# Optimization experiments

Hardware: AMD Instinct MI355X
Metric: run time of the kernel (lower is better)

The kernel has to match this reference:

```python
import jax, jax.numpy as jnp
import numpy as np

B, N, C, R = 16, 1024, 256, 8
E = 262144
NUM_SUPER = 32
EPS = 1e-5


def _ln(x, g, b):
    mu = jnp.mean(x, axis=-1, keepdims=True)
    var = jnp.var(x, axis=-1, keepdims=True)
    return (x - mu) / jnp.sqrt(var + EPS) * g + b


def setup_inputs() -> dict:
    key = jax.random.key(0)
    ks = jax.random.split(key, 20)

    def w(k, shape, fan_in):
        return (jax.random.normal(k, shape, jnp.float32) / np.sqrt(fan_in)).astype(jnp.float32)

    return dict(
        x=jax.random.normal(ks[0], (B, N, C), jnp.float32),
        batch_edge_index=jax.random.randint(ks[1], (2, E), 0, B * N),
        batch_edge_types=jax.random.randint(ks[2], (E,), 0, R),
        # cross-modal attention
        Wq=w(ks[3], (C, C), C), bq=jnp.zeros((C,), jnp.float32),
        Wk=w(ks[4], (C, C), C), bk=jnp.zeros((C,), jnp.float32),
        Wv=w(ks[5], (C, C), C), bv=jnp.zeros((C,), jnp.float32),
        Wg=w(ks[6], (2 * C, C), 2 * C), bg=jnp.zeros((C,), jnp.float32),
        ln_attn_g=jnp.ones((C,), jnp.float32), ln_attn_b=jnp.zeros((C,), jnp.float32),
        # confidence net
        Wc1=w(ks[7], (C, C // 2), C), bc1=jnp.zeros((C // 2,), jnp.float32),
        Wc2=w(ks[8], (C // 2, 1), C // 2), bc2=jnp.zeros((1,), jnp.float32),
        # feature mixer
        Wm=w(ks[9], (2 * C, C), 2 * C), bm=jnp.zeros((C,), jnp.float32),
        ln1_g=jnp.ones((C,), jnp.float32), ln1_b=jnp.zeros((C,), jnp.float32),
        # RGCN
        W_rel=w(ks[10], (R, C, C), C),
        W_root=w(ks[11], (C, C), C),
        b_rgcn=jnp.zeros((C,), jnp.float32),
        ln2_g=jnp.ones((C,), jnp.float32), ln2_b=jnp.zeros((C,), jnp.float32),
        # super class head
        Wh=w(ks[12], (C, NUM_SUPER), C), bh=jnp.zeros((NUM_SUPER,), jnp.float32),
    )


def reference(x, batch_edge_index, batch_edge_types,
              Wq, bq, Wk, bk, Wv, bv, Wg, bg, ln_attn_g, ln_attn_b,
              Wc1, bc1, Wc2, bc2, Wm, bm, ln1_g, ln1_b,
              W_rel, W_root, b_rgcn, ln2_g, ln2_b, Wh, bh):
    residual = x
    q = x @ Wq + bq
    k = x @ Wk + bk
    v = x @ Wv + bv
    attn = jax.nn.softmax(jnp.einsum('bnc,bmc->bnm', q, k) / jnp.sqrt(jnp.float32(C)), axis=-1)
    out = jnp.einsum('bnm,bmc->bnc', attn, v)
    gate = jax.nn.sigmoid(jnp.concatenate([out, residual], axis=-1) @ Wg + bg)
    validated = _ln(gate * out + (1.0 - gate) * residual, ln_attn_g, ln_attn_b)

    conf = jax.nn.sigmoid(jax.nn.relu(validated @ Wc1 + bc1) @ Wc2 + bc2)  # [B,N,1]
    weighted = validated * conf
    xm = jax.nn.relu(jnp.concatenate([x, weighted], axis=-1) @ Wm + bm)
    xn = _ln(xm, ln1_g, ln1_b).reshape(B * N, C)

    # RGCNConv (PyG defaults: mean aggregation per relation, root weight, bias)
    src, dst = batch_edge_index[0], batch_edge_index[1]
    h = jnp.einsum('nc,rcd->rnd', xn, W_rel)          # [R, B*N, C] relation-transformed nodes
    msg = h[batch_edge_types, src]                    # [E, C] per-edge gather
    seg = dst * R + batch_edge_types                  # (node, relation) segment id
    cnt = jax.ops.segment_sum(jnp.ones((E,), xn.dtype), seg, num_segments=B * N * R)
    msg = msg / jnp.maximum(cnt[seg], 1.0)[:, None]
    agg = jax.ops.segment_sum(msg, dst, num_segments=B * N)
    x_rgcn = agg + xn @ W_root + b_rgcn
    x_rgcn = jax.nn.relu(_ln(x_rgcn.reshape(B, N, C), ln2_g, ln2_b))

    denom = jnp.maximum(conf.sum(axis=1), 1e-8)       # [B,1]
    pooled = (x_rgcn * conf).sum(axis=1) / denom      # [B,C]
    return pooled @ Wh + bh                           # [B, NUM_SUPER]
```

## Files before the change

### kernel.cpp

```cpp
#include <hip/hip_runtime.h>
#include <hip/hip_bf16.h>

#define B_ 16
#define N_ 1024
#define C_ 256
#define R_ 8
#define E_ 262144
#define NS_ 32
#define BN_ (B_*N_)
#define BNC_ (BN_*C_)

typedef __hip_bfloat16 bf16;
typedef __attribute__((ext_vector_type(4))) float f32x4;
typedef __attribute__((ext_vector_type(8))) short bf16x8;

__device__ __forceinline__ float b2f(bf16 x) { return __bfloat162float(x); }
__device__ __forceinline__ bf16  f2b(float x) { return __float2bfloat16(x); }
__device__ __forceinline__ float us2f(unsigned short u) { return __uint_as_float((unsigned)u << 16); }

__device__ __forceinline__ void gload16(const void* g, void* l) {
    auto gp = (const __attribute__((address_space(1))) void*)(unsigned long long)g;
    auto lp = (__attribute__((address_space(3))) void*)(unsigned)(unsigned long long)l;
    __builtin_amdgcn_global_load_lds(gp, lp, 16, 0, 0);
}

template<int ACT>
__global__ __launch_bounds__(256) void gemm_bf16(
    const bf16* __restrict__ A, int lda, long long sA,
    const bf16* __restrict__ Bm, int ldb, long long sB,
    bf16* __restrict__ Cc, int ldc, long long sC,
    const float* __restrict__ bias, const float* __restrict__ bias2,
    const float* __restrict__ bias3, int K)
{
    __shared__ short sbuf[16384];
    const int tid = threadIdx.x;
    const int lane = tid & 63, w = tid >> 6;
    const int wr = w >> 1, wc = w & 1;
    const int bm = blockIdx.y * 128, bn = blockIdx.x * 128;
    const bf16* Ab = A + (size_t)blockIdx.z * sA;
    const bf16* Bb = Bm + (size_t)blockIdx.z * sB;
    bf16* Cb = Cc + (size_t)blockIdx.z * sC;

    const int rg = lane >> 2;
    const int kswz = ((lane & 3) ^ ((rg >> 1) & 3)) * 8;

    f32x4 acc[4][4];
    const f32x4 zz = {0.f, 0.f, 0.f, 0.f};
    #pragma unroll
    for (int i = 0; i < 4; ++i)
        #pragma unroll
        for (int j = 0; j < 4; ++j) acc[i][j] = zz;

    const int fr = lane & 15;
    const int fm = lane >> 4;
    const int fslot = (fm ^ ((fr >> 1) & 3)) * 8;

    const int NI = K >> 5;

#define STAGE_AB(bi, kk) do {                                                          \
    _Pragma("unroll")                                                                  \
    for (int t_ = 0; t_ < 2; ++t_) {                                                   \
        gload16(Ab + (size_t)(bm + t_*64 + w*16 + rg) * lda + (kk) + kswz,             \
                sbuf + (bi)*4096 + t_*2048 + w*512);                                   \
        gload16(Bb + (size_t)(bn + t_*64 + w*16 + rg) * ldb + (kk) + kswz,             \
                sbuf + 8192 + (bi)*4096 + t_*2048 + w*512);                            \
    } } while (0)

    STAGE_AB(0, 0);
    if (NI > 1) STAGE_AB(1, 32);

    for (int i = 0; i < NI; ++i) {
        const int cur = i & 1;
        if (i + 1 < NI) asm volatile("s_waitcnt vmcnt(4)" ::: "memory");
        else            asm volatile("s_waitcnt vmcnt(0)" ::: "memory");
        __builtin_amdgcn_s_barrier();
        __builtin_amdgcn_sched_barrier(0);

        bf16x8 af[4], bfr[4];
        const short* Ac = sbuf + cur * 4096;
        const short* Bc = sbuf + 8192 + cur * 4096;
        #pragma unroll
        for (int ii = 0; ii < 4; ++ii)
            af[ii] = *(const bf16x8*)&Ac[(wr*64 + ii*16 + fr)*32 + fslot];
        #pragma unroll
        for (int jj = 0; jj < 4; ++jj)
            bfr[jj] = *(const bf16x8*)&Bc[(wc*64 + jj*16 + fr)*32 + fslot];

        asm volatile("s_waitcnt lgkmcnt(0)" ::: "memory");
        __builtin_amdgcn_s_barrier();
        __builtin_amdgcn_sched_barrier(0);
        if (i + 2 < NI) STAGE_AB(cur, (i + 2) * 32);

        #pragma unroll
        for (int ii = 0; ii < 4; ++ii)
            #pragma unroll
            for (int jj = 0; jj < 4; ++jj)
                acc[ii][jj] = __builtin_amdgcn_mfma_f32_16x16x32_bf16(af[ii], bfr[jj], acc[ii][jj], 0, 0, 0);
    }
#undef STAGE_AB

    __syncthreads();
    const int er = (lane >> 4) * 4, ec = lane & 15;
    #pragma unroll
    for (int half = 0; half < 2; ++half) {
        if (wr == half) {
            #pragma unroll
            for (int j = 0; j < 4; ++j) {
                const int col = bn + wc*64 + j*16 + ec;
                float bvv = 0.0f;
                if (bias) {
                    const int seg = col >> 8;
                    const float* bp = (seg == 0) ? bias : (seg == 1 ? bias2 : bias3);
                    bvv = bp[col & 255];
                }
                #pragma unroll
                for (int i = 0; i < 4; ++i) {
                    #pragma unroll
                    for (int p = 0; p < 4; ++p) {
                        float val = acc[i][j][p] + bvv;
                        if (ACT == 1) val = fmaxf(val, 0.0f);
                        if (ACT == 2) val = 1.0f / (1.0f + __expf(-val));
                        *(bf16*)&sbuf[(i*16 + er + p)*136 + wc*64 + j*16 + ec] = f2b(val);
                    }
                }
            }
        }
        __syncthreads();
        #pragma unroll
        for (int it = 0; it < 4; ++it) {
            const int ch = tid + it*256;
            const int row = ch >> 4, cp = (ch & 15) * 8;
            *(bf16x8*)&Cb[(size_t)(bm + half*64 + row) * ldc + bn + cp] =
                *(const bf16x8*)&sbuf[row*136 + cp];
        }
        __syncthreads();
    }
}

template<int ACT>
__global__ __launch_bounds__(256) void gemm64_bf16(
    const bf16* __restrict__ A, int lda, long long sA,
    const bf16* __restrict__ Bm, int ldb, long long sB,
    bf16* __restrict__ Cc, int ldc, long long sC,
    const float* __restrict__ bias, int K)
{
    __shared__ short sbuf[8192];
    const int tid = threadIdx.x;
    const int lane = tid & 63, w = tid >> 6;
    const int wr = w >> 1, wc = w & 1;
    const int bm = blockIdx.y * 64, bn = blockIdx.x * 64;
    const bf16* Ab = A + (size_t)blockIdx.z * sA;
    const bf16* Bb = Bm + (size_t)blockIdx.z * sB;
    bf16* Cb = Cc + (size_t)blockIdx.z * sC;

    const int rg = lane >> 2;
    const int kswz = ((lane & 3) ^ ((rg >> 1) & 3)) * 8;

    f32x4 acc[2][2];
    const f32x4 zz = {0.f, 0.f, 0.f, 0.f};
    #pragma unroll
    for (int i = 0; i < 2; ++i)
        #pragma unroll
        for (int j = 0; j < 2; ++j) acc[i][j] = zz;

    const int fr = lane & 15;
    const int fm = lane >> 4;
    const int fslot = (fm ^ ((fr >> 1) & 3)) * 8;

    const int NI = K >> 5;

#define STAGE64(bi, kk) do {                                                           \
    gload16(Ab + (size_t)(bm + w*16 + rg) * lda + (kk) + kswz,                         \
            sbuf + (bi)*2048 + w*512);                                                 \
    gload16(Bb + (size_t)(bn + w*16 + rg) * ldb + (kk) + kswz,                         \
            sbuf + 4096 + (bi)*2048 + w*512);                                          \
    } while (0)

    STAGE64(0, 0);
    if (NI > 1) STAGE64(1, 32);

    for (int i = 0; i < NI; ++i) {
        const int cur = i & 1;
        if (i + 1 < NI) asm volatile("s_waitcnt vmcnt(2)" ::: "memory");
        else            asm volatile("s_waitcnt vmcnt(0)" ::: "memory");
        __builtin_amdgcn_s_barrier();
        __builtin_amdgcn_sched_barrier(0);

        bf16x8 af[2], bfr[2];
        const short* Ac = sbuf + cur * 2048;
        const short* Bc = sbuf + 4096 + cur * 2048;
        #pragma unroll
        for (int ii = 0; ii < 2; ++ii)
            af[ii] = *(const bf16x8*)&Ac[(wr*32 + ii*16 + fr)*32 + fslot];
        #pragma unroll
        for (int jj = 0; jj < 2; ++jj)
            bfr[jj] = *(const bf16x8*)&Bc[(wc*32 + jj*16 + fr)*32 + fslot];

        asm volatile("s_waitcnt lgkmcnt(0)" ::: "memory");
        __builtin_amdgcn_s_barrier();
        __builtin_amdgcn_sched_barrier(0);
        if (i + 2 < NI) STAGE64(cur, (i + 2) * 32);

        #pragma unroll
        for (int ii = 0; ii < 2; ++ii)
            #pragma unroll
            for (int jj = 0; jj < 2; ++jj)
                acc[ii][jj] = __builtin_amdgcn_mfma_f32_16x16x32_bf16(af[ii], bfr[jj], acc[ii][jj], 0, 0, 0);
    }
#undef STAGE64

    __syncthreads();
    const int er = (lane >> 4) * 4, ec = lane & 15;
    #pragma unroll
    for (int j = 0; j < 2; ++j) {
        const int col = bn + wc*32 + j*16 + ec;
        const float bvv = bias ? bias[col & 255] : 0.0f;
        #pragma unroll
        for (int i = 0; i < 2; ++i) {
            #pragma unroll
            for (int p = 0; p < 4; ++p) {
                float val = acc[i][j][p] + bvv;
                if (ACT == 1) val = fmaxf(val, 0.0f);
                if (ACT == 2) val = 1.0f / (1.0f + __expf(-val));
                *(bf16*)&sbuf[(wr*32 + i*16 + er + p)*72 + wc*32 + j*16 + ec] = f2b(val);
            }
        }
    }
    __syncthreads();
    #pragma unroll
    for (int it = 0; it < 2; ++it) {
        const int ch = tid + it*256;
        const int row = ch >> 3, cp = (ch & 7) * 8;
        *(bf16x8*)&Cb[(size_t)(bm + row) * ldc + bn + cp] =
            *(const bf16x8*)&sbuf[row*72 + cp];
    }
}

__global__ __launch_bounds__(256) void prep_w_k(
    const float* __restrict__ Wq, const float* __restrict__ Wk, const float* __restrict__ Wv,
    const float* __restrict__ Wg, const float* __restrict__ Wm, const float* __restrict__ Wc1,
    const float* __restrict__ Wrel, const float* __restrict__ Wroot, bf16* __restrict__ WT)
{
    int t = blockIdx.x;
    const float* in; bf16* out; int K, Nn;
    if (t < 192)      { int wsel = t >> 6; t &= 63;
                        in = wsel == 0 ? Wq : (wsel == 1 ? Wk : Wv);
                        out = WT + wsel*65536; K = 256; Nn = 256; }
    else if (t < 320) { t -= 192; in = Wg;  out = WT + 196608; K = 512; Nn = 256; }
    else if (t < 448) { t -= 320; in = Wm;  out = WT + 327680; K = 512; Nn = 256; }
    else if (t < 480) { t -= 448; in = Wc1; out = WT + 458752; K = 256; Nn = 128; }
    else if (t < 992) { t -= 480; int r = t >> 6; t &= 63;
                        in = Wrel + (size_t)r*65536; out = WT + 491520 + r*65536; K = 256; Nn = 256; }
    else              { t -= 992; in = Wroot; out = WT + 491520 + 524288; K = 256; Nn = 256; }
    const int tpr = Nn >> 5;
    const int n0 = (t % tpr) * 32, k0 = (t / tpr) * 32;
    __shared__ float tile[32][33];
    const int tx = threadIdx.x & 31, ty = threadIdx.x >> 5;
    #pragma unroll
    for (int i = 0; i < 4; ++i) {
        int r = ty + i*8;
        tile[r][tx] = in[(size_t)(k0 + r) * Nn + n0 + tx];
    }
    __syncthreads();
    #pragma unroll
    for (int i = 0; i < 4; ++i) {
        int r = ty + i*8;
        out[(size_t)(n0 + r) * K + k0 + tx] = f2b(tile[tx][r]);
    }
}

__global__ __launch_bounds__(256) void vtrans_k(
    const bf16* __restrict__ in, bf16* __restrict__ out)
{
    __shared__ float tile[32][33];
    in  += (size_t)blockIdx.z * 786432 + 512;
    out += (size_t)blockIdx.z * 262144;
    const int n0 = blockIdx.x * 32, k0 = blockIdx.y * 32;
    const int tx = threadIdx.x & 31, ty = threadIdx.x >> 5;
    #pragma unroll
    for (int i = 0; i < 4; ++i) {
        int r = ty + i*8;
        tile[r][tx] = b2f(in[(size_t)(k0 + r) * 768 + n0 + tx]);
    }
    __syncthreads();
    #pragma unroll
    for (int i = 0; i < 4; ++i) {
        int r = ty + i*8;
        out[(size_t)(n0 + r) * 1024 + k0 + tx] = f2b(tile[tx][r]);
    }
}

__global__ __launch_bounds__(256) void cvt_x_k(const float* __restrict__ x,
    bf16* __restrict__ xb, bf16* __restrict__ cat1, bf16* __restrict__ cat2)
{
    const int i4 = (blockIdx.x * 256 + threadIdx.x) * 4;
    const float4 xv = *(const float4*)(x + i4);
    bf16 bv[4] = { f2b(xv.x), f2b(xv.y), f2b(xv.z), f2b(xv.w) };
    const ushort4 pack = *(const ushort4*)bv;
    const int row = i4 >> 8, col = i4 & 255;
    *(ushort4*)(xb + i4) = pack;
    *(ushort4*)(cat1 + (size_t)row * 512 + 256 + col) = pack;
    *(ushort4*)(cat2 + (size_t)row * 512 + col) = pack;
}

__global__ __launch_bounds__(256) void softmax_k(bf16* __restrict__ s)
{
    const int row = blockIdx.x, tid = threadIdx.x;
    const int lane = tid & 63, wid = tid >> 6;
    bf16* rp = s + (size_t)row * 1024 + tid * 4;
    __shared__ float red[8];
    const ushort4 sv = *(const ushort4*)rp;
    float v0 = us2f(sv.x) * 0.0625f, v1 = us2f(sv.y) * 0.0625f;
    float v2 = us2f(sv.z) * 0.0625f, v3 = us2f(sv.w) * 0.0625f;
    float m = fmaxf(fmaxf(v0, v1), fmaxf(v2, v3));
    #pragma unroll
    for (int o = 32; o >= 1; o >>= 1) m = fmaxf(m, __shfl_xor(m, o));
    if (lane == 0) red[wid] = m;
    __syncthreads();
    const float mx = fmaxf(fmaxf(red[0], red[1]), fmaxf(red[2], red[3]));
    float e0 = __expf(v0 - mx), e1 = __expf(v1 - mx), e2 = __expf(v2 - mx), e3 = __expf(v3 - mx);
    float sm = e0 + e1 + e2 + e3;
    #pragma unroll
    for (int o = 32; o >= 1; o >>= 1) sm += __shfl_xor(sm, o);
    if (lane == 0) red[4 + wid] = sm;
    __syncthreads();
    const float inv = 1.0f / (red[4] + red[5] + red[6] + red[7]);
    bf16 ov[4] = { f2b(e0 * inv), f2b(e1 * inv), f2b(e2 * inv), f2b(e3 * inv) };
    *(ushort4*)rp = *(const ushort4*)ov;
}

template<int RELU>
__global__ __launch_bounds__(256) void ln_k(
    const bf16* __restrict__ in, bf16* __restrict__ out,
    const float* __restrict__ g, const float* __restrict__ bta)
{
    const int node = blockIdx.x * 4 + (threadIdx.x >> 6);
    const int lane = threadIdx.x & 63;
    const ushort4 iv = *(const ushort4*)(in + (size_t)node * 256 + lane * 4);
    float v0 = us2f(iv.x), v1 = us2f(iv.y), v2 = us2f(iv.z), v3 = us2f(iv.w);
    float s  = v0 + v1 + v2 + v3;
    float sq = v0*v0 + v1*v1 + v2*v2 + v3*v3;
    #pragma unroll
    for (int o = 32; o >= 1; o >>= 1) { s += __shfl_xor(s, o); sq += __shfl_xor(sq, o); }
    const float mean = s * (1.0f / 256.0f);
    const float var  = sq * (1.0f / 256.0f) - mean * mean;
    const float rs = rsqrtf(var + 1e-5f);
    const float4 gv = *(const float4*)(g + lane * 4);
    const float4 bv = *(const float4*)(bta + lane * 4);
    float y0 = (v0 - mean) * rs * gv.x + bv.x;
    float y1 = (v1 - mean) * rs * gv.y + bv.y;
    float y2 = (v2 - mean) * rs * gv.z + bv.z;
    float y3 = (v3 - mean) * rs * gv.w + bv.w;
    if (RELU) { y0 = fmaxf(y0, 0.f); y1 = fmaxf(y1, 0.f); y2 = fmaxf(y2, 0.f); y3 = fmaxf(y3, 0.f); }
    bf16 ov[4] = { f2b(y0), f2b(y1), f2b(y2), f2b(y3) };
    *(ushort4*)(out + (size_t)node * 256 + lane * 4) = *(const ushort4*)ov;
}

__global__ __launch_bounds__(256) void blend_ln_k(
    const bf16* __restrict__ gate, const bf16* __restrict__ cat1,
    const float* __restrict__ x, bf16* __restrict__ valid,
    const float* __restrict__ g, const float* __restrict__ bta)
{
    const int node = blockIdx.x * 4 + (threadIdx.x >> 6);
    const int lane = threadIdx.x & 63;
    const ushort4 gt4 = *(const ushort4*)(gate + (size_t)node * 256 + lane * 4);
    const ushort4 ao4 = *(const ushort4*)(cat1 + (size_t)node * 512 + lane * 4);
    const float4  xv4 = *(const float4*)(x + (size_t)node * 256 + lane * 4);
    float g0 = us2f(gt4.x), g1 = us2f(gt4.y), g2 = us2f(gt4.z), g3 = us2f(gt4.w);
    float v0 = g0 * us2f(ao4.x) + (1.f - g0) * xv4.x;
    float v1 = g1 * us2f(ao4.y) + (1.f - g1) * xv4.y;
    float v2 = g2 * us2f(ao4.z) + (1.f - g2) * xv4.z;
    float v3 = g3 * us2f(ao4.w) + (1.f - g3) * xv4.w;
    float s  = v0 + v1 + v2 + v3;
    float sq = v0*v0 + v1*v1 + v2*v2 + v3*v3;
    #pragma unroll
    for (int o = 32; o >= 1; o >>= 1) { s += __shfl_xor(s, o); sq += __shfl_xor(sq, o); }
    const float mean = s * (1.0f / 256.0f);
    const float var  = sq * (1.0f / 256.0f) - mean * mean;
    const float rs = rsqrtf(var + 1e-5f);
    const float4 gv = *(const float4*)(g + lane * 4);
    const float4 bv = *(const float4*)(bta + lane * 4);
    bf16 ov[4] = { f2b((v0 - mean) * rs * gv.x + bv.x), f2b((v1 - mean) * rs * gv.y + bv.y),
                   f2b((v2 - mean) * rs * gv.z + bv.z), f2b((v3 - mean) * rs * gv.w + bv.w) };
    *(ushort4*)(valid + (size_t)node * 256 + lane * 4) = *(const ushort4*)ov;
}

__global__ __launch_bounds__(256) void conf_w_k(
    const bf16* __restrict__ t1, const float* __restrict__ Wc2, const float* __restrict__ bc2,
    const bf16* __restrict__ valid, float* __restrict__ conf, bf16* __restrict__ cat2)
{
    const int node = blockIdx.x * 4 + (threadIdx.x >> 6);
    const int lane = threadIdx.x & 63;
    float a = b2f(t1[(size_t)node * 128 + lane]) * Wc2[lane]
            + b2f(t1[(size_t)node * 128 + 64 + lane]) * Wc2[64 + lane];
    #pragma unroll
    for (int o = 32; o >= 1; o >>= 1) a += __shfl_xor(a, o);
    const float c = 1.0f / (1.0f + __expf(-(a + bc2[0])));
    if (lane == 0) conf[node] = c;
    const ushort4 vv = *(const ushort4*)(valid + (size_t)node * 256 + lane * 4);
    bf16 ov[4] = { f2b(us2f(vv.x) * c), f2b(us2f(vv.y) * c), f2b(us2f(vv.z) * c), f2b(us2f(vv.w) * c) };
    *(ushort4*)(cat2 + (size_t)node * 512 + 256 + lane * 4) = *(const ushort4*)ov;
}

__global__ __launch_bounds__(256) void count2_k(
    const int* __restrict__ dst, const int* __restrict__ et,
    int* __restrict__ deg, int* __restrict__ cnt8)
{
    const int e = blockIdx.x * 256 + threadIdx.x;
    if (e < E_) {
        const int d = dst[e];
        atomicAdd(&deg[d], 1);
        atomicAdd(&cnt8[d * 8 + et[e]], 1);
    }
}

__global__ __launch_bounds__(256) void scan_k(
    const int* __restrict__ deg, int* __restrict__ rowptr, int* __restrict__ cursor)
{
    __shared__ int part[256];
    const int tid = threadIdx.x;
    const int base = tid * 64;
    int s = 0;
    for (int i = 0; i < 64; ++i) s += deg[base + i];
    part[tid] = s; __syncthreads();
    for (int off = 1; off < 256; off <<= 1) {
        int t = (tid >= off) ? part[tid - off] : 0;
        __syncthreads();
        part[tid] += t;
        __syncthreads();
    }
    int run = (tid == 0) ? 0 : part[tid - 1];
    for (int i = 0; i < 64; ++i) {
        rowptr[base + i] = run;
        cursor[base + i] = run;
        run += deg[base + i];
    }
    if (tid == 255) rowptr[BN_] = run;
}

__global__ __launch_bounds__(256) void fill_k(
    const int* __restrict__ src, const int* __restrict__ dst, const int* __restrict__ et,
    int* __restrict__ cursor, int* __restrict__ elist)
{
    const int e = blockIdx.x * 256 + threadIdx.x;
    if (e < E_) {
        const int pos = atomicAdd(&cursor[dst[e]], 1);
        elist[pos] = src[e] | (et[e] << 16);
    }
}

__global__ __launch_bounds__(256) void gather_ln_k(
    const int* __restrict__ rowptr, const int* __restrict__ elist,
    const bf16* __restrict__ h, const int* __restrict__ cnt8,
    const float* __restrict__ brg,
    const float* __restrict__ g, const float* __restrict__ bta,
    bf16* __restrict__ xr)
{
    const int node = blockIdx.x * 4 + (threadIdx.x >> 6);
    const int lane = threadIdx.x & 63;
    const int e0 = rowptr[node], e1 = rowptr[node + 1];
    float invc[8];
    #pragma unroll
    for (int r = 0; r < 8; ++r)
        invc[r] = 1.0f / fmaxf((float)cnt8[node * 8 + r], 1.0f);
    float a0 = 0.f, a1 = 0.f, a2 = 0.f, a3 = 0.f;
    for (int e = e0; e < e1; ++e) {
        const int pe = elist[e];
        const int srcn = pe & 0xffff, rel = pe >> 16;
        const float wgt = invc[rel];
        const ushort4 hv = *(const ushort4*)(h + (size_t)srcn * 2304 + rel * 256 + lane * 4);
        a0 += wgt * us2f(hv.x); a1 += wgt * us2f(hv.y);
        a2 += wgt * us2f(hv.z); a3 += wgt * us2f(hv.w);
    }
    const ushort4 rv = *(const ushort4*)(h + (size_t)node * 2304 + 2048 + lane * 4);
    const float4 bg4 = *(const float4*)(brg + lane * 4);
    const float v0 = a0 + us2f(rv.x) + bg4.x, v1 = a1 + us2f(rv.y) + bg4.y;
    const float v2 = a2 + us2f(rv.z) + bg4.z, v3 = a3 + us2f(rv.w) + bg4.w;
    float s  = v0 + v1 + v2 + v3;
    float sq = v0*v0 + v1*v1 + v2*v2 + v3*v3;
    #pragma unroll
    for (int m = 32; m >= 1; m >>= 1) { s += __shfl_xor(s, m); sq += __shfl_xor(sq, m); }
    const float mean = s * (1.0f / 256.0f);
    const float var  = sq * (1.0f / 256.0f) - mean * mean;
    const float rs = rsqrtf(var + 1e-5f);
    const float4 gv = *(const float4*)(g + lane * 4);
    const float4 bv = *(const float4*)(bta + lane * 4);
    bf16 tb[4] = { f2b(fmaxf((v0 - mean) * rs * gv.x + bv.x, 0.f)),
                   f2b(fmaxf((v1 - mean) * rs * gv.y + bv.y, 0.f)),
                   f2b(fmaxf((v2 - mean) * rs * gv.z + bv.z, 0.f)),
                   f2b(fmaxf((v3 - mean) * rs * gv.w + bv.w, 0.f)) };
    *(ushort4*)(xr + (size_t)node * 256 + lane * 4) = *(const ushort4*)tb;
}

__global__ __launch_bounds__(256) void pool1_k(
    const bf16* __restrict__ xr, const float* __restrict__ conf, float* __restrict__ partial)
{
    const int b = blockIdx.x, chunk = blockIdx.y, c = threadIdx.x;
    float acc = 0.0f;
    for (int n = 0; n < 64; ++n) {
        const int node = b * 1024 + chunk * 64 + n;
        acc += conf[node] * b2f(xr[(size_t)node * 256 + c]);
    }
    partial[(size_t)(b * 16 + chunk) * 256 + c] = acc;
}

__global__ __launch_bounds__(256) void pool2_k(
    const float* __restrict__ partial, const float* __restrict__ conf,
    const float* __restrict__ Wh, const float* __restrict__ bh, float* __restrict__ out)
{
    const int b = blockIdx.x, tid = threadIdx.x;
    __shared__ float red[256];
    __shared__ float pooled[256];
    float pc = 0.0f;
    for (int ch = 0; ch < 16; ++ch) pc += partial[(size_t)(b * 16 + ch) * 256 + tid];
    float s = conf[b * 1024 + tid] + conf[b * 1024 + 256 + tid]
            + conf[b * 1024 + 512 + tid] + conf[b * 1024 + 768 + tid];
    red[tid] = s; __syncthreads();
    for (int st = 128; st > 0; st >>= 1) { if (tid < st) red[tid] += red[tid + st]; __syncthreads(); }
    const float denom = fmaxf(red[0], 1e-8f);
    pooled[tid] = pc / denom;
    __syncthreads();
    if (tid < NS_) {
        float o = bh[tid];
        for (int c = 0; c < 256; ++c) o += pooled[c] * Wh[c * NS_ + tid];
        out[b * NS_ + tid] = o;
    }
}

extern "C" void kernel_launch(void* const* d_in, const int* in_sizes, int n_in,
                              void* d_out, int out_size, void* d_ws, size_t ws_size,
                              hipStream_t stream) {
    const float* x    = (const float*)d_in[0];
    const int*   ei   = (const int*)d_in[1];
    const int*   et   = (const int*)d_in[2];
    const float* Wq   = (const float*)d_in[3];  const float* bq  = (const float*)d_in[4];
    const float* Wk   = (const float*)d_in[5];  const float* bk  = (const float*)d_in[6];
    const float* Wv   = (const float*)d_in[7];  const float* bv  = (const float*)d_in[8];
    const float* Wg   = (const float*)d_in[9];  const float* bg  = (const float*)d_in[10];
    const float* lag  = (const float*)d_in[11]; const float* lab = (const float*)d_in[12];
    const float* Wc1  = (const float*)d_in[13]; const float* bc1 = (const float*)d_in[14];
    const float* Wc2  = (const float*)d_in[15]; const float* bc2 = (const float*)d_in[16];
    const float* Wm   = (const float*)d_in[17]; const float* bm  = (const float*)d_in[18];
    const float* l1g  = (const float*)d_in[19]; const float* l1b = (const float*)d_in[20];
    const float* Wrel = (const float*)d_in[21]; const float* Wroot = (const float*)d_in[22];
    const float* brg  = (const float*)d_in[23];
    const float* l2g  = (const float*)d_in[24]; const float* l2b = (const float*)d_in[25];
    const float* Wh   = (const float*)d_in[26]; const float* bh  = (const float*)d_in[27];
    const int* esrc = ei;
    const int* edst = ei + E_;

    char* w8 = (char*)d_ws;
    bf16*  qkv   = (bf16*)(w8 + 0);
    bf16*  hbuf  = (bf16*)(w8 + 0);
    bf16*  sP    = (bf16*)(w8 + 25165824);
    bf16*  cat1  = (bf16*)(w8 + 58720256);
    bf16*  cat2  = (bf16*)(w8 + 75497472);
    bf16*  gate  = (bf16*)(w8 + 92274688);
    bf16*  valid = (bf16*)(w8 + 100663296);
    bf16*  t1    = (bf16*)(w8 + 109051904);
    bf16*  xm    = (bf16*)(w8 + 113246208);
    bf16*  xb    = (bf16*)(w8 + 121634816);
    bf16*  xn    = (bf16*)(w8 + 130023424);
    bf16*  vtb   = (bf16*)(w8 + 138412032);
    bf16*  xr    = (bf16*)(w8 + 146800640);
    float* conf  = (float*)(w8 + 155189248);
    float* part  = (float*)(w8 + 155254784);
    bf16*  WT    = (bf16*)(w8 + 155516928);
    int*  deg    = (int*)(w8 + 157679616);
    int*  cnt8i  = (int*)(w8 + 157745152);
    int*  rowptr = (int*)(w8 + 158269440);
    int*  cursor = (int*)(w8 + 158335232);
    int*  elist  = (int*)(w8 + 158400768);
    bf16* WqkvT = WT;
    bf16* WgT   = WT + 196608;
    bf16* WmT   = WT + 327680;
    bf16* Wc1T  = WT + 458752;
    bf16* WBIG  = WT + 491520;
    float* outp = (float*)d_out;

    dim3 blk(256);

    prep_w_k<<<1056, blk, 0, stream>>>(Wq, Wk, Wv, Wg, Wm, Wc1, Wrel, Wroot, WT);
    cvt_x_k<<<BNC_ / 1024, blk, 0, stream>>>(x, xb, cat1, cat2);
    hipMemsetAsync(deg, 0, 589824, stream);
    count2_k<<<E_ / 256, blk, 0, stream>>>(edst, et, deg, cnt8i);
    scan_k<<<1, blk, 0, stream>>>(deg, rowptr, cursor);
    fill_k<<<E_ / 256, blk, 0, stream>>>(esrc, edst, et, cursor, elist);

    gemm_bf16<0><<<dim3(6, 128, 1), blk, 0, stream>>>(
        xb, 256, 0, WqkvT, 256, 0, qkv, 768, 0, bq, bk, bv, 256);
    vtrans_k<<<dim3(8, 32, 16), blk, 0, stream>>>(qkv, vtb);

    gemm_bf16<0><<<dim3(8, 8, 16), blk, 0, stream>>>(
        qkv, 768, 786432, qkv + 256, 768, 786432, sP, 1024, 1048576, nullptr, nullptr, nullptr, 256);
    softmax_k<<<BN_, blk, 0, stream>>>(sP);
    gemm64_bf16<0><<<dim3(4, 16, 16), blk, 0, stream>>>(
        sP, 1024, 1048576, vtb, 1024, 262144, cat1, 512, 524288, nullptr, 1024);

    gemm64_bf16<2><<<dim3(4, 256, 1), blk, 0, stream>>>(
        cat1, 512, 0, WgT, 512, 0, gate, 256, 0, bg, 512);
    blend_ln_k<<<BN_ / 4, blk, 0, stream>>>(gate, cat1, x, valid, lag, lab);

    gemm64_bf16<1><<<dim3(2, 256, 1), blk, 0, stream>>>(
        valid, 256, 0, Wc1T, 256, 0, t1, 128, 0, bc1, 256);
    conf_w_k<<<BN_ / 4, blk, 0, stream>>>(t1, Wc2, bc2, valid, conf, cat2);

    gemm64_bf16<1><<<dim3(4, 256, 1), blk, 0, stream>>>(
        cat2, 512, 0, WmT, 512, 0, xm, 256, 0, bm, 512);
    ln_k<0><<<BN_ / 4, blk, 0, stream>>>(xm, xn, l1g, l1b);

    gemm_bf16<0><<<dim3(18, 128, 1), blk, 0, stream>>>(
        xn, 256, 0, WBIG, 256, 0, hbuf, 2304, 0, nullptr, nullptr, nullptr, 256);
    gather_ln_k<<<BN_ / 4, blk, 0, stream>>>(rowptr, elist, hbuf, cnt8i, brg, l2g, l2b, xr);

    pool1_k<<<dim3(B_, 16), blk, 0, stream>>>(xr, conf, part);
    pool2_k<<<B_, blk, 0, stream>>>(part, conf, Wh, bh, outp);
}
```

Before: 289.2 us.

## Fuse QK^T, softmax and PV into a flash-attention style kernel

Replaces the three-stage attention (score GEMM writing a 16x1024x1024 bf16 matrix, a separate softmax pass, then the PV GEMM) with a single kernel that keeps scores in registers and applies an online softmax with running max and sum. Each wave handles 16 query rows and half of the output channels, reading K and V fragments straight from global memory with no LDS staging, and passing P through LDS to reshape it into MFMA operands. This removes the round trips of the large score matrix through HBM and two kernel launches. In exchange K and V are re-read by every wave without shared tiling, the grid is only 512 blocks, and the score computation is duplicated across the two channel-half waves.

```diff
diff --git a/kernel.cpp b/kernel.cpp
--- a/kernel.cpp
+++ b/kernel.cpp
@@ -16,6 +16,7 @@
 
 __device__ __forceinline__ float b2f(bf16 x) { return __bfloat162float(x); }
 __device__ __forceinline__ bf16  f2b(float x) { return __float2bfloat16(x); }
+__device__ __forceinline__ unsigned short f2bu(float x) { bf16 b = f2b(x); return *(unsigned short*)&b; }
 __device__ __forceinline__ float us2f(unsigned short u) { return __uint_as_float((unsigned)u << 16); }
 
 __device__ __forceinline__ void gload16(const void* g, void* l) {
@@ -236,6 +237,123 @@
     }
 }
 
+__global__ __launch_bounds__(256) void attn_k(
+    const bf16* __restrict__ qkv, const bf16* __restrict__ vtb, bf16* __restrict__ outc)
+{
+    __shared__ short pbuf[4096];
+    __shared__ short ebuf[8704];
+    const int tid = threadIdx.x;
+    const int lane = tid & 63, w = tid >> 6;
+    const int qg = w >> 1, ch = w & 1;
+    const int batch = blockIdx.y;
+    const int qbase = blockIdx.x * 32 + qg * 16;
+    const bf16* Qb = qkv + (size_t)batch * 786432;
+    const bf16* Kb = Qb + 256;
+    const bf16* Vb = vtb + (size_t)batch * 262144;
+    const int fr = lane & 15, fg = lane >> 4;
+    short* Pw = pbuf + w * 1024;
+    short* Ew = ebuf + w * 2176;
+
+    bf16x8 qf[8];
+    #pragma unroll
+    for (int c = 0; c < 8; ++c)
+        qf[c] = *(const bf16x8*)(Qb + (size_t)(qbase + fr) * 768 + c*32 + fg*8);
+
+    f32x4 o[8];
+    #pragma unroll
+    for (int i = 0; i < 8; ++i) o[i] = (f32x4){0.f, 0.f, 0.f, 0.f};
+    float m_run = -INFINITY, l_run = 0.0f;
+
+    for (int kt = 0; kt < 16; ++kt) {
+        f32x4 st[4];
+        #pragma unroll
+        for (int kf = 0; kf < 4; ++kf) {
+            st[kf] = (f32x4){0.f, 0.f, 0.f, 0.f};
+            #pragma unroll
+            for (int c = 0; c < 8; ++c) {
+                bf16x8 kfrag = *(const bf16x8*)(Kb + (size_t)(kt*64 + kf*16 + fr) * 768 + c*32 + fg*8);
+                st[kf] = __builtin_amdgcn_mfma_f32_16x16x32_bf16(kfrag, qf[c], st[kf], 0, 0, 0);
+            }
+        }
+        float tm = -INFINITY;
+        #pragma unroll
+        for (int kf = 0; kf < 4; ++kf)
+            #pragma unroll
+            for (int r = 0; r < 4; ++r) {
+                st[kf][r] *= 0.0625f;
+                tm = fmaxf(tm, st[kf][r]);
+            }
+        tm = fmaxf(tm, __shfl_xor(tm, 16));
+        tm = fmaxf(tm, __shfl_xor(tm, 32));
+        const float m_new = fmaxf(m_run, tm);
+        const float sf = __expf(m_run - m_new);
+        float ts = 0.0f;
+        float p[16];
+        #pragma unroll
+        for (int kf = 0; kf < 4; ++kf)
+            #pragma unroll
+            for (int r = 0; r < 4; ++r) {
+                const float e = __expf(st[kf][r] - m_new);
+                p[kf*4 + r] = e; ts += e;
+            }
+        ts += __shfl_xor(ts, 16);
+        ts += __shfl_xor(ts, 32);
+        l_run = l_run * sf + ts;
+        m_run = m_new;
+        float sfr[4];
+        #pragma unroll
+        for (int r = 0; r < 4; ++r) sfr[r] = __shfl(sf, fg*4 + r);
+        #pragma unroll
+        for (int cf = 0; cf < 8; ++cf)
+            #pragma unroll
+            for (int r = 0; r < 4; ++r) o[cf][r] *= sfr[r];
+        asm volatile("s_waitcnt lgkmcnt(0)" ::: "memory");
+        #pragma unroll
+        for (int kf = 0; kf < 4; ++kf) {
+            const int oswz = (kf*2 + (fg>>1)) ^ ((fr>>1)&3);
+            #pragma unroll
+            for (int rp = 0; rp < 2; ++rp) {
+                const unsigned pk = (unsigned)f2bu(p[kf*4 + rp*2])
+                                  | ((unsigned)f2bu(p[kf*4 + rp*2 + 1]) << 16);
+                ((unsigned*)Pw)[fr*32 + oswz*4 + (fg&1)*2 + rp] = pk;
+            }
+        }
+        asm volatile("s_waitcnt lgkmcnt(0)" ::: "memory");
+        __builtin_amdgcn_sched_barrier(0);
+        bf16x8 pa[2];
+        #pragma unroll
+        for (int ks = 0; ks < 2; ++ks)
+            pa[ks] = *(const bf16x8*)&Pw[fr*64 + (((ks*4 + fg) ^ ((fr>>1)&3)))*8];
+        asm volatile("s_waitcnt lgkmcnt(0)" ::: "memory");
+        __builtin_amdgcn_sched_barrier(0);
+        #pragma unroll
+        for (int cf = 0; cf < 8; ++cf)
+            #pragma unroll
+            for (int ks = 0; ks < 2; ++ks) {
+                bf16x8 vfrag = *(const bf16x8*)(Vb + (size_t)(ch*128 + cf*16 + fr) * 1024 + kt*64 + ks*32 + fg*8);
+                o[cf] = __builtin_amdgcn_mfma_f32_16x16x32_bf16(pa[ks], vfrag, o[cf], 0, 0, 0);
+            }
+    }
+
+    float linv[4];
+    #pragma unroll
+    for (int r = 0; r < 4; ++r) linv[r] = 1.0f / __shfl(l_run, fg*4 + r);
+    #pragma unroll
+    for (int cf = 0; cf < 8; ++cf)
+        #pragma unroll
+        for (int r = 0; r < 4; ++r)
+            Ew[(fg*4 + r)*136 + cf*16 + fr] = (short)f2bu(o[cf][r] * linv[r]);
+    asm volatile("s_waitcnt lgkmcnt(0)" ::: "memory");
+    __builtin_amdgcn_sched_barrier(0);
+    #pragma unroll
+    for (int it = 0; it < 4; ++it) {
+        const int cidx = it*64 + lane;
+        const int row = cidx >> 4, cp = (cidx & 15) * 8;
+        *(bf16x8*)&outc[(size_t)(batch*1024 + qbase + row) * 512 + ch*128 + cp] =
+            *(const bf16x8*)&Ew[row*136 + cp];
+    }
+}
+
 __global__ __launch_bounds__(256) void prep_w_k(
     const float* __restrict__ Wq, const float* __restrict__ Wk, const float* __restrict__ Wv,
     const float* __restrict__ Wg, const float* __restrict__ Wm, const float* __restrict__ Wc1,
@@ -301,32 +419,6 @@
     *(ushort4*)(xb + i4) = pack;
     *(ushort4*)(cat1 + (size_t)row * 512 + 256 + col) = pack;
     *(ushort4*)(cat2 + (size_t)row * 512 + col) = pack;
-}
-
-__global__ __launch_bounds__(256) void softmax_k(bf16* __restrict__ s)
-{
-    const int row = blockIdx.x, tid = threadIdx.x;
-    const int lane = tid & 63, wid = tid >> 6;
-    bf16* rp = s + (size_t)row * 1024 + tid * 4;
-    __shared__ float red[8];
-    const ushort4 sv = *(const ushort4*)rp;
-    float v0 = us2f(sv.x) * 0.0625f, v1 = us2f(sv.y) * 0.0625f;
-    float v2 = us2f(sv.z) * 0.0625f, v3 = us2f(sv.w) * 0.0625f;
-    float m = fmaxf(fmaxf(v0, v1), fmaxf(v2, v3));
-    #pragma unroll
-    for (int o = 32; o >= 1; o >>= 1) m = fmaxf(m, __shfl_xor(m, o));
-    if (lane == 0) red[wid] = m;
-    __syncthreads();
-    const float mx = fmaxf(fmaxf(red[0], red[1]), fmaxf(red[2], red[3]));
-    float e0 = __expf(v0 - mx), e1 = __expf(v1 - mx), e2 = __expf(v2 - mx), e3 = __expf(v3 - mx);
-    float sm = e0 + e1 + e2 + e3;
-    #pragma unroll
-    for (int o = 32; o >= 1; o >>= 1) sm += __shfl_xor(sm, o);
-    if (lane == 0) red[4 + wid] = sm;
-    __syncthreads();
-    const float inv = 1.0f / (red[4] + red[5] + red[6] + red[7]);
-    bf16 ov[4] = { f2b(e0 * inv), f2b(e1 * inv), f2b(e2 * inv), f2b(e3 * inv) };
-    *(ushort4*)rp = *(const ushort4*)ov;
 }
 
 template<int RELU>
@@ -552,7 +644,6 @@
     char* w8 = (char*)d_ws;
     bf16*  qkv   = (bf16*)(w8 + 0);
     bf16*  hbuf  = (bf16*)(w8 + 0);
-    bf16*  sP    = (bf16*)(w8 + 25165824);
     bf16*  cat1  = (bf16*)(w8 + 58720256);
     bf16*  cat2  = (bf16*)(w8 + 75497472);
     bf16*  gate  = (bf16*)(w8 + 92274688);
@@ -591,11 +682,7 @@
         xb, 256, 0, WqkvT, 256, 0, qkv, 768, 0, bq, bk, bv, 256);
     vtrans_k<<<dim3(8, 32, 16), blk, 0, stream>>>(qkv, vtb);
 
-    gemm_bf16<0><<<dim3(8, 8, 16), blk, 0, stream>>>(
-        qkv, 768, 786432, qkv + 256, 768, 786432, sP, 1024, 1048576, nullptr, nullptr, nullptr, 256);
-    softmax_k<<<BN_, blk, 0, stream>>>(sP);
-    gemm64_bf16<0><<<dim3(4, 16, 16), blk, 0, stream>>>(
-        sP, 1024, 1048576, vtb, 1024, 262144, cat1, 512, 524288, nullptr, 1024);
+    attn_k<<<dim3(32, 16), blk, 0, stream>>>(qkv, vtb, cat1);
 
     gemm64_bf16<2><<<dim3(4, 256, 1), blk, 0, stream>>>(
         cat1, 512, 0, WgT, 512, 0, gate, 256, 0, bg, 512);
```

After: 395.1 us. 1.37x slower.
